# Optimization experiments

Hardware: AMD Instinct MI355X
Metric: run time of the kernel (lower is better)

## Reference

```python
import jax, jax.numpy as jnp
import numpy as np

TOP_K = 2  # config.top_k


def setup_inputs() -> dict:
    key = jax.random.key(0)
    k0, k1, k2, k3, k4 = jax.random.split(key, 5)
    B, S, D, F, E = 1, 2048, 512, 1024, 8
    scale = 0.02
    hidden_states = jax.random.normal(k0, (B, S, D), dtype=jnp.float32)
    router_w = jax.random.normal(k1, (D, E), dtype=jnp.float32) * scale
    w1 = jax.random.normal(k2, (E, D, F), dtype=jnp.float32) * scale  # gate proj
    w2 = jax.random.normal(k3, (E, F, D), dtype=jnp.float32) * scale  # down proj
    w3 = jax.random.normal(k4, (E, D, F), dtype=jnp.float32) * scale  # up proj
    return {"hidden_states": hidden_states, "router_w": router_w,
            "w1": w1, "w2": w2, "w3": w3}


def reference(hidden_states, router_w, w1, w2, w3):
    B, S, D = hidden_states.shape
    E = router_w.shape[1]
    x = hidden_states.reshape(-1, D)                      # [T, D]
    T = x.shape[0]

    # router: softmax in float32, top-k, renormalize (matches torch source)
    router_logits = x @ router_w                          # [T, E]
    probs = jax.nn.softmax(router_logits.astype(jnp.float32), axis=-1)
    routing_weights, selected_experts = jax.lax.top_k(probs, TOP_K)  # [T, K]
    routing_weights = routing_weights / routing_weights.sum(axis=-1, keepdims=True)
    routing_weights = routing_weights.astype(x.dtype)

    # combine weights: scatter top-k weights into dense [T, E] (one-hot combine)
    combine = jnp.zeros((T, E), dtype=x.dtype).at[
        jnp.arange(T)[:, None], selected_experts].add(routing_weights)

    # dense-all-experts evaluation, math-identical to gather-GEMM-scatter:
    # unselected experts get combine weight 0 and contribute nothing.
    gate = jax.nn.silu(jnp.einsum('td,edf->tef', x, w1))  # [T, E, F]
    up = jnp.einsum('td,edf->tef', x, w3)                 # [T, E, F]
    h = gate * up * combine[:, :, None]                   # weight before down-proj
    out = jnp.einsum('tef,efd->td', h, w2)                # [T, D]
    return out.reshape(B, S, D)
```

## Files before the change

kernel.cpp:

```cpp
#include <hip/hip_runtime.h>
#include <hip/hip_bf16.h>


typedef __attribute__((ext_vector_type(4))) float f32x4;
typedef __attribute__((ext_vector_type(8))) __bf16 bf16x8;

#define T_TOK 2048
#define DMODEL 512
#define FFN 1024
#define NE 8
#define MAXMB 40
#define PCAP (MAXMB * 128)

__device__ __forceinline__ void gload_lds16(const void* g, void* l) {
  __builtin_amdgcn_global_load_lds(
      (const __attribute__((address_space(1))) void*)g,
      (__attribute__((address_space(3))) void*)l, 16, 0, 0);
}

#define PIPE_BAR_8()                                        \
  asm volatile("s_waitcnt vmcnt(8)" ::: "memory");          \
  __builtin_amdgcn_s_barrier();                             \
  __builtin_amdgcn_sched_barrier(0)
#define PIPE_BAR_6()                                        \
  asm volatile("s_waitcnt vmcnt(6)" ::: "memory");          \
  __builtin_amdgcn_s_barrier();                             \
  __builtin_amdgcn_sched_barrier(0)
#define PIPE_BAR_0()                                        \
  asm volatile("s_waitcnt vmcnt(0)" ::: "memory");          \
  __builtin_amdgcn_s_barrier();                             \
  __builtin_amdgcn_sched_barrier(0)
#define POST_BAR()                                          \
  __builtin_amdgcn_s_barrier();                             \
  __builtin_amdgcn_sched_barrier(0)

__global__ __launch_bounds__(256) void cvt_router_kernel(
    const float* __restrict__ x, const float* __restrict__ rw,
    __bf16* __restrict__ xb, int* __restrict__ tope, float* __restrict__ topw) {
  const int t = blockIdx.x * 4 + (threadIdx.x >> 6);
  const int lane = threadIdx.x & 63;
  const float* xr = x + (size_t)t * DMODEL + lane * 8;
  const f32x4 a = *(const f32x4*)xr;
  const f32x4 b = *(const f32x4*)(xr + 4);
  bf16x8 v;
  v[0] = (__bf16)a[0]; v[1] = (__bf16)a[1]; v[2] = (__bf16)a[2]; v[3] = (__bf16)a[3];
  v[4] = (__bf16)b[0]; v[5] = (__bf16)b[1]; v[6] = (__bf16)b[2]; v[7] = (__bf16)b[3];
  *(bf16x8*)&xb[(size_t)t * DMODEL + lane * 8] = v;

  float xv[8] = {a[0], a[1], a[2], a[3], b[0], b[1], b[2], b[3]};
  float part[NE];
#pragma unroll
  for (int e = 0; e < NE; ++e) part[e] = 0.f;
#pragma unroll
  for (int i = 0; i < 8; ++i) {
    const int d = lane * 8 + i;
    const f32x4 r0 = *(const f32x4*)&rw[(size_t)d * NE];
    const f32x4 r1 = *(const f32x4*)&rw[(size_t)d * NE + 4];
    part[0] += xv[i] * r0[0]; part[1] += xv[i] * r0[1];
    part[2] += xv[i] * r0[2]; part[3] += xv[i] * r0[3];
    part[4] += xv[i] * r1[0]; part[5] += xv[i] * r1[1];
    part[6] += xv[i] * r1[2]; part[7] += xv[i] * r1[3];
  }
#pragma unroll
  for (int off = 32; off > 0; off >>= 1) {
#pragma unroll
    for (int e = 0; e < NE; ++e) part[e] += __shfl_xor(part[e], off);
  }
  if (lane == 0) {
    int ia = 0;
#pragma unroll
    for (int e = 1; e < NE; ++e)
      if (part[e] > part[ia]) ia = e;
    int ib = (ia == 0) ? 1 : 0;
#pragma unroll
    for (int e = 0; e < NE; ++e)
      if (e != ia && e != ib && part[e] > part[ib]) ib = e;
    const float wa = 1.f / (1.f + __expf(part[ib] - part[ia]));
    tope[t * 2] = ia;
    tope[t * 2 + 1] = ib;
    topw[t * 2] = wa;
    topw[t * 2 + 1] = 1.f - wa;
  }
}

__global__ __launch_bounds__(256) void build_kernel(
    const int* __restrict__ tope, const float* __restrict__ topw,
    int* __restrict__ pair_t, float* __restrict__ pair_w,
    int* __restrict__ pairidx, int* __restrict__ sched_e) {
  __shared__ int cnt[NE], base[NE], ofs[NE];
  const int tid = threadIdx.x;
  if (tid < NE) { cnt[tid] = 0; ofs[tid] = 0; }
  for (int i = tid; i < PCAP; i += 256) { pair_t[i] = 0; pair_w[i] = 0.f; }
  for (int i = tid; i < MAXMB; i += 256) sched_e[i] = -1;
  __syncthreads();
  for (int t = tid; t < T_TOK; t += 256) {
    atomicAdd(&cnt[tope[t * 2]], 1);
    atomicAdd(&cnt[tope[t * 2 + 1]], 1);
  }
  __syncthreads();
  if (tid == 0) {
    int mb = 0;
    for (int e = 0; e < NE; ++e) {
      base[e] = mb * 128;
      const int nmb = (cnt[e] + 127) >> 7;
      for (int i = 0; i < nmb; ++i) sched_e[mb + i] = e;
      mb += nmb;
    }
  }
  __syncthreads();
  for (int t = tid; t < T_TOK; t += 256) {
#pragma unroll
    for (int s = 0; s < 2; ++s) {
      const int e = tope[t * 2 + s];
      const int pos = base[e] + atomicAdd(&ofs[e], 1);
      pair_t[pos] = t;
      pair_w[pos] = topw[t * 2 + s];
      pairidx[t * 2 + s] = pos;
    }
  }
}

__global__ __launch_bounds__(256) void transpose_all_kernel(
    const float* __restrict__ w1, const float* __restrict__ w2,
    const float* __restrict__ w3, __bf16* __restrict__ w1t,
    __bf16* __restrict__ w2t, __bf16* __restrict__ w3t) {
  __shared__ __bf16 tile[64][65];
  const int tid = threadIdx.x;
  const int bx = blockIdx.x;
  const float* src;
  __bf16* dst;
  int R, C, idx;
  if (bx < 1024)      { src = w1; dst = w1t; R = 512;  C = 1024; idx = bx; }
  else if (bx < 2048) { src = w3; dst = w3t; R = 512;  C = 1024; idx = bx - 1024; }
  else                { src = w2; dst = w2t; R = 1024; C = 512;  idx = bx - 2048; }
  const int ntx = C >> 6, nty = R >> 6;
  const int cx = idx % ntx;
  const int gry = idx / ntx;
  const int e = gry / nty;
  const int r0 = (gry % nty) * 64;
  const int c0 = cx * 64;
  src += (size_t)e * R * C;
  dst += (size_t)e * R * C;
#pragma unroll
  for (int q = 0; q < 4; ++q) {
    const int r = (tid >> 4) + q * 16;
    const int c = (tid & 15) * 4;
    const f32x4 v = *(const f32x4*)&src[(size_t)(r0 + r) * C + c0 + c];
    tile[r][c] = (__bf16)v[0];
    tile[r][c + 1] = (__bf16)v[1];
    tile[r][c + 2] = (__bf16)v[2];
    tile[r][c + 3] = (__bf16)v[3];
  }
  __syncthreads();
#pragma unroll
  for (int p = 0; p < 2; ++p) {
    const int cc = (tid >> 3) + p * 32;
    const int rr = (tid & 7) * 8;
    union { bf16x8 v; __bf16 s[8]; } u;
#pragma unroll
    for (int i = 0; i < 8; ++i) u.s[i] = tile[rr + i][cc];
    *(bf16x8*)&dst[(size_t)(c0 + cc) * R + r0 + rr] = u.v;
  }
}

__global__ __launch_bounds__(256) void gemm1_kernel(
    const __bf16* __restrict__ xb, const __bf16* __restrict__ w1t,
    const __bf16* __restrict__ w3t, const int* __restrict__ pair_t,
    const float* __restrict__ pair_w, const int* __restrict__ sched_e,
    __bf16* __restrict__ hbuf) {
  __shared__ alignas(16) __bf16 As[2][128 * 64];
  __shared__ alignas(16) __bf16 B1s[2][64 * 64];
  __shared__ alignas(16) __bf16 B3s[2][64 * 64];
  __shared__ float comb[128];
  const int tid = threadIdx.x;
  const int id = blockIdx.x;
  const int mb = (id & 7) + ((id >> 7) << 3);
  const int f0 = ((id >> 3) & 15) * 64;
  const int e = sched_e[mb];
  if (e < 0) return;
  const int m0 = mb * 128;
  const int lane = tid & 63;
  const int wv = tid >> 6;
  const int wr = wv >> 1, wc = wv & 1;
  const int l15 = lane & 15, lhi = lane >> 4;
  const int sw = (l15 & 7) << 4;

  if (tid < 128) comb[tid] = pair_w[m0 + tid];

  size_t aoff[4];
  int lbA[4];
#pragma unroll
  for (int it = 0; it < 4; ++it) {
    const int chunk = it * 256 + tid;
    const int r = chunk >> 3;
    const int c8 = ((chunk & 7) ^ (r & 7)) * 8;
    aoff[it] = (size_t)pair_t[m0 + r] * DMODEL + c8;
    lbA[it] = (it * 256 + (tid & ~63)) * 16;
  }
  size_t boff[2];
  int lbB[2];
#pragma unroll
  for (int it = 0; it < 2; ++it) {
    const int chunk = it * 256 + tid;
    const int r = chunk >> 3;
    const int c8 = ((chunk & 7) ^ (r & 7)) * 8;
    boff[it] = (size_t)(e * FFN + f0 + r) * DMODEL + c8;
    lbB[it] = (it * 256 + (tid & ~63)) * 16;
  }

  const f32x4 fz = {0.f, 0.f, 0.f, 0.f};
  f32x4 acc1[4][2], acc3[4][2];
#pragma unroll
  for (int m = 0; m < 4; ++m)
#pragma unroll
    for (int n = 0; n < 2; ++n) { acc1[m][n] = fz; acc3[m][n] = fz; }

#define G1_STAGE(BUF, K0)                                                     \
  do {                                                                        \
    _Pragma("unroll") for (int it = 0; it < 4; ++it)                          \
        gload_lds16(xb + aoff[it] + (K0), (char*)As[BUF] + lbA[it]);          \
    _Pragma("unroll") for (int it = 0; it < 2; ++it) {                        \
      gload_lds16(w1t + boff[it] + (K0), (char*)B1s[BUF] + lbB[it]);          \
      gload_lds16(w3t + boff[it] + (K0), (char*)B3s[BUF] + lbB[it]);          \
    }                                                                         \
  } while (0)

#define G1_COMPUTE(BUF)                                                       \
  do {                                                                        \
    __builtin_amdgcn_s_setprio(1);                                            \
    _Pragma("unroll") for (int kk = 0; kk < 2; ++kk) {                        \
      const int ko = (kk * 64 + lhi * 16) ^ sw;                               \
      bf16x8 af[4], b1f[2], b3f[2];                                           \
      _Pragma("unroll") for (int m = 0; m < 4; ++m)                           \
          af[m] = *(const bf16x8*)((const char*)As[BUF] +                     \
                                   (wr * 64 + m * 16 + l15) * 128 + ko);      \
      _Pragma("unroll") for (int n = 0; n < 2; ++n) {                         \
        const int ro = (wc * 32 + n * 16 + l15) * 128 + ko;                   \
        b1f[n] = *(const bf16x8*)((const char*)B1s[BUF] + ro);                \
        b3f[n] = *(const bf16x8*)((const char*)B3s[BUF] + ro);                \
      }                                                                       \
      _Pragma("unroll") for (int m = 0; m < 4; ++m)                           \
          _Pragma("unroll") for (int n = 0; n < 2; ++n) {                     \
        acc1[m][n] = __builtin_amdgcn_mfma_f32_16x16x32_bf16(af[m], b1f[n],   \
                                                             acc1[m][n], 0, 0, 0); \
        acc3[m][n] = __builtin_amdgcn_mfma_f32_16x16x32_bf16(af[m], b3f[n],   \
                                                             acc3[m][n], 0, 0, 0); \
      }                                                                       \
    }                                                                         \
    __builtin_amdgcn_s_setprio(0);                                            \
  } while (0)

  G1_STAGE(0, 0);
#pragma unroll
  for (int t = 0; t < 7; ++t) {
    G1_STAGE((t + 1) & 1, (t + 1) * 64);
    PIPE_BAR_8();
    G1_COMPUTE(t & 1);
    POST_BAR();
  }
  PIPE_BAR_0();
  G1_COMPUTE(1);

#pragma unroll
  for (int m = 0; m < 4; ++m)
#pragma unroll
    for (int n = 0; n < 2; ++n)
#pragma unroll
      for (int r = 0; r < 4; ++r) {
        const int row = wr * 64 + m * 16 + lhi * 4 + r;
        const int col = wc * 32 + n * 16 + l15;
        const float g = acc1[m][n][r];
        const float u = acc3[m][n][r];
        const float val = (g / (1.f + __expf(-g))) * u * comb[row];
        hbuf[(size_t)(m0 + row) * FFN + f0 + col] = (__bf16)val;
      }
#undef G1_STAGE
#undef G1_COMPUTE
}

__global__ __launch_bounds__(256) void gemm2_kernel(
    const __bf16* __restrict__ hbuf, const __bf16* __restrict__ w2t,
    const int* __restrict__ sched_e, __bf16* __restrict__ outp) {
  __shared__ alignas(16) __bf16 As[2][128 * 64];
  __shared__ alignas(16) __bf16 Bs[2][64 * 64];
  const int tid = threadIdx.x;
  const int id = blockIdx.x;
  const int gk = (id & 7) + ((id >> 6) << 3);
  const int n0 = ((id >> 3) & 7) * 64;
  const int mb = gk >> 1;
  const int kz = gk & 1;
  const int e = sched_e[mb];
  if (e < 0) return;
  const int m0 = mb * 128;
  const int fbase = kz * (FFN / 2);
  const int lane = tid & 63;
  const int wv = tid >> 6;
  const int wr = wv >> 1, wc = wv & 1;
  const int l15 = lane & 15, lhi = lane >> 4;
  const int sw = (l15 & 7) << 4;

  size_t aoff[4];
  int lbA[4];
#pragma unroll
  for (int it = 0; it < 4; ++it) {
    const int chunk = it * 256 + tid;
    const int r = chunk >> 3;
    const int c8 = ((chunk & 7) ^ (r & 7)) * 8;
    aoff[it] = (size_t)(m0 + r) * FFN + fbase + c8;
    lbA[it] = (it * 256 + (tid & ~63)) * 16;
  }
  size_t boff[2];
  int lbB[2];
#pragma unroll
  for (int it = 0; it < 2; ++it) {
    const int chunk = it * 256 + tid;
    const int r = chunk >> 3;
    const int c8 = ((chunk & 7) ^ (r & 7)) * 8;
    boff[it] = ((size_t)e * DMODEL + n0 + r) * FFN + fbase + c8;
    lbB[it] = (it * 256 + (tid & ~63)) * 16;
  }

  const f32x4 fz = {0.f, 0.f, 0.f, 0.f};
  f32x4 acc[4][2];
#pragma unroll
  for (int m = 0; m < 4; ++m) { acc[m][0] = fz; acc[m][1] = fz; }

#define G2_STAGE(BUF, K0)                                                     \
  do {                                                                        \
    _Pragma("unroll") for (int it = 0; it < 4; ++it)                          \
        gload_lds16(hbuf + aoff[it] + (K0), (char*)As[BUF] + lbA[it]);        \
    _Pragma("unroll") for (int it = 0; it < 2; ++it)                          \
        gload_lds16(w2t + boff[it] + (K0), (char*)Bs[BUF] + lbB[it]);         \
  } while (0)

#define G2_COMPUTE(BUF)                                                       \
  do {                                                                        \
    __builtin_amdgcn_s_setprio(1);                                            \
    _Pragma("unroll") for (int kk = 0; kk < 2; ++kk) {                        \
      const int ko = (kk * 64 + lhi * 16) ^ sw;                               \
      bf16x8 af[4], bfr[2];                                                   \
      _Pragma("unroll") for (int m = 0; m < 4; ++m)                           \
          af[m] = *(const bf16x8*)((const char*)As[BUF] +                     \
                                   (wr * 64 + m * 16 + l15) * 128 + ko);      \
      _Pragma("unroll") for (int n = 0; n < 2; ++n)                           \
          bfr[n] = *(const bf16x8*)((const char*)Bs[BUF] +                    \
                                    (wc * 32 + n * 16 + l15) * 128 + ko);     \
      _Pragma("unroll") for (int m = 0; m < 4; ++m)                           \
          _Pragma("unroll") for (int n = 0; n < 2; ++n)                       \
              acc[m][n] = __builtin_amdgcn_mfma_f32_16x16x32_bf16(            \
                  af[m], bfr[n], acc[m][n], 0, 0, 0);                         \
    }                                                                         \
    __builtin_amdgcn_s_setprio(0);                                            \
  } while (0)

  G2_STAGE(0, 0);
#pragma unroll
  for (int t = 0; t < 7; ++t) {
    G2_STAGE((t + 1) & 1, (t + 1) * 64);
    PIPE_BAR_6();
    G2_COMPUTE(t & 1);
    POST_BAR();
  }
  PIPE_BAR_0();
  G2_COMPUTE(1);

#pragma unroll
  for (int m = 0; m < 4; ++m)
#pragma unroll
    for (int n = 0; n < 2; ++n)
#pragma unroll
      for (int r = 0; r < 4; ++r) {
        const int row = wr * 64 + m * 16 + lhi * 4 + r;
        const int col = wc * 32 + n * 16 + l15;
        outp[((size_t)kz * PCAP + m0 + row) * DMODEL + n0 + col] =
            (__bf16)acc[m][n][r];
      }
#undef G2_STAGE
#undef G2_COMPUTE
}

__global__ __launch_bounds__(256) void gather_kernel(
    const __bf16* __restrict__ outp, const int* __restrict__ pairidx,
    float* __restrict__ out) {
  const int i = blockIdx.x * 256 + threadIdx.x;
  const int t = i >> 6;
  const int c = (i & 63) * 8;
  const int p0 = pairidx[t * 2];
  const int p1 = pairidx[t * 2 + 1];
  const size_t KZ = (size_t)PCAP * DMODEL;
  const bf16x8 a0 = *(const bf16x8*)&outp[(size_t)p0 * DMODEL + c];
  const bf16x8 a1 = *(const bf16x8*)&outp[(size_t)p1 * DMODEL + c];
  const bf16x8 b0 = *(const bf16x8*)&outp[KZ + (size_t)p0 * DMODEL + c];
  const bf16x8 b1 = *(const bf16x8*)&outp[KZ + (size_t)p1 * DMODEL + c];
  f32x4 lo, hi;
#pragma unroll
  for (int j = 0; j < 4; ++j)
    lo[j] = (float)a0[j] + (float)a1[j] + (float)b0[j] + (float)b1[j];
#pragma unroll
  for (int j = 0; j < 4; ++j)
    hi[j] = (float)a0[j + 4] + (float)a1[j + 4] + (float)b0[j + 4] + (float)b1[j + 4];
  float* op = out + (size_t)t * DMODEL + c;
  *(f32x4*)op = lo;
  *(f32x4*)(op + 4) = hi;
}

extern "C" void kernel_launch(void* const* d_in, const int* in_sizes, int n_in,
                              void* d_out, int out_size, void* d_ws, size_t ws_size,
                              hipStream_t stream) {
  const float* x = (const float*)d_in[0];
  const float* rw = (const float*)d_in[1];
  const float* w1 = (const float*)d_in[2];
  const float* w2 = (const float*)d_in[3];
  const float* w3 = (const float*)d_in[4];
  float* out = (float*)d_out;
  char* ws = (char*)d_ws;

  int* tope = (int*)(ws + 0);
  float* topw = (float*)(ws + 16384);
  int* pair_t = (int*)(ws + 32768);
  float* pair_w = (float*)(ws + 53248);
  int* pairidx = (int*)(ws + 73728);
  int* sched_e = (int*)(ws + 90112);
  __bf16* xb = (__bf16*)(ws + 98304);
  __bf16* w1t = (__bf16*)(ws + 2195456);
  __bf16* w3t = (__bf16*)(ws + 10584064);
  __bf16* w2t = (__bf16*)(ws + 18972672);
  __bf16* hbuf = (__bf16*)(ws + 27361280);
  __bf16* outp = (__bf16*)(ws + 37847040);

  hipLaunchKernelGGL(cvt_router_kernel, dim3(T_TOK / 4), dim3(256), 0, stream, x, rw, xb, tope, topw);
  hipLaunchKernelGGL(build_kernel, dim3(1), dim3(256), 0, stream, tope, topw, pair_t, pair_w, pairidx, sched_e);
  hipLaunchKernelGGL(transpose_all_kernel, dim3(3072), dim3(256), 0, stream, w1, w2, w3, w1t, w2t, w3t);
  hipLaunchKernelGGL(gemm1_kernel, dim3(640), dim3(256), 0, stream, xb, w1t, w3t, pair_t, pair_w, sched_e, hbuf);
  hipLaunchKernelGGL(gemm2_kernel, dim3(640), dim3(256), 0, stream, hbuf, w2t, sched_e, outp);
  hipLaunchKernelGGL(gather_kernel, dim3(512), dim3(256), 0, stream, outp, pairidx, out);
}
```

Baseline: 74.09 us.

## Fuse router, weight transpose and init into one prep kernel; stage GEMM epilogues via LDS

Merges the router/convert kernel, the weight transpose kernel and the pair-buffer initialization into a single prep kernel. This removes one launch and moves the serial init loop out of the single-block build kernel. Both GEMM epilogues now write results to a padded LDS tile first and then store 16-byte vectors to global memory, replacing scattered 2-byte writes. The costs are an extra barrier plus LDS round trip per tile, and a larger, more divergent prep kernel.

```diff
diff --git a/kernel.cpp b/kernel.cpp
--- a/kernel.cpp
+++ b/kernel.cpp
@@ -34,52 +34,102 @@
   __builtin_amdgcn_s_barrier();                             \
   __builtin_amdgcn_sched_barrier(0)
 
-__global__ __launch_bounds__(256) void cvt_router_kernel(
+__global__ __launch_bounds__(256) void prep_kernel(
     const float* __restrict__ x, const float* __restrict__ rw,
-    __bf16* __restrict__ xb, int* __restrict__ tope, float* __restrict__ topw) {
-  const int t = blockIdx.x * 4 + (threadIdx.x >> 6);
-  const int lane = threadIdx.x & 63;
-  const float* xr = x + (size_t)t * DMODEL + lane * 8;
-  const f32x4 a = *(const f32x4*)xr;
-  const f32x4 b = *(const f32x4*)(xr + 4);
-  bf16x8 v;
-  v[0] = (__bf16)a[0]; v[1] = (__bf16)a[1]; v[2] = (__bf16)a[2]; v[3] = (__bf16)a[3];
-  v[4] = (__bf16)b[0]; v[5] = (__bf16)b[1]; v[6] = (__bf16)b[2]; v[7] = (__bf16)b[3];
-  *(bf16x8*)&xb[(size_t)t * DMODEL + lane * 8] = v;
-
-  float xv[8] = {a[0], a[1], a[2], a[3], b[0], b[1], b[2], b[3]};
-  float part[NE];
-#pragma unroll
-  for (int e = 0; e < NE; ++e) part[e] = 0.f;
-#pragma unroll
-  for (int i = 0; i < 8; ++i) {
-    const int d = lane * 8 + i;
-    const f32x4 r0 = *(const f32x4*)&rw[(size_t)d * NE];
-    const f32x4 r1 = *(const f32x4*)&rw[(size_t)d * NE + 4];
-    part[0] += xv[i] * r0[0]; part[1] += xv[i] * r0[1];
-    part[2] += xv[i] * r0[2]; part[3] += xv[i] * r0[3];
-    part[4] += xv[i] * r1[0]; part[5] += xv[i] * r1[1];
-    part[6] += xv[i] * r1[2]; part[7] += xv[i] * r1[3];
-  }
-#pragma unroll
-  for (int off = 32; off > 0; off >>= 1) {
-#pragma unroll
-    for (int e = 0; e < NE; ++e) part[e] += __shfl_xor(part[e], off);
-  }
-  if (lane == 0) {
-    int ia = 0;
-#pragma unroll
-    for (int e = 1; e < NE; ++e)
-      if (part[e] > part[ia]) ia = e;
-    int ib = (ia == 0) ? 1 : 0;
-#pragma unroll
-    for (int e = 0; e < NE; ++e)
-      if (e != ia && e != ib && part[e] > part[ib]) ib = e;
-    const float wa = 1.f / (1.f + __expf(part[ib] - part[ia]));
-    tope[t * 2] = ia;
-    tope[t * 2 + 1] = ib;
-    topw[t * 2] = wa;
-    topw[t * 2 + 1] = 1.f - wa;
+    const float* __restrict__ w1, const float* __restrict__ w2,
+    const float* __restrict__ w3, __bf16* __restrict__ xb,
+    __bf16* __restrict__ w1t, __bf16* __restrict__ w2t,
+    __bf16* __restrict__ w3t, int* __restrict__ tope, float* __restrict__ topw,
+    int* __restrict__ pair_t, float* __restrict__ pair_w,
+    int* __restrict__ sched_e) {
+  __shared__ __bf16 tile[64][65];
+  const int bx = blockIdx.x;
+  const int tid = threadIdx.x;
+
+  if (bx < 3072) {
+    const float* src;
+    __bf16* dst;
+    int R, C, idx;
+    if (bx < 1024)      { src = w1; dst = w1t; R = 512;  C = 1024; idx = bx; }
+    else if (bx < 2048) { src = w3; dst = w3t; R = 512;  C = 1024; idx = bx - 1024; }
+    else                { src = w2; dst = w2t; R = 1024; C = 512;  idx = bx - 2048; }
+    const int ntx = C >> 6, nty = R >> 6;
+    const int cx = idx % ntx;
+    const int gry = idx / ntx;
+    const int e = gry / nty;
+    const int r0 = (gry % nty) * 64;
+    const int c0 = cx * 64;
+    src += (size_t)e * R * C;
+    dst += (size_t)e * R * C;
+#pragma unroll
+    for (int q = 0; q < 4; ++q) {
+      const int r = (tid >> 4) + q * 16;
+      const int c = (tid & 15) * 4;
+      const f32x4 v = *(const f32x4*)&src[(size_t)(r0 + r) * C + c0 + c];
+      tile[r][c] = (__bf16)v[0];
+      tile[r][c + 1] = (__bf16)v[1];
+      tile[r][c + 2] = (__bf16)v[2];
+      tile[r][c + 3] = (__bf16)v[3];
+    }
+    __syncthreads();
+#pragma unroll
+    for (int p = 0; p < 2; ++p) {
+      const int cc = (tid >> 3) + p * 32;
+      const int rr = (tid & 7) * 8;
+      union { bf16x8 v; __bf16 s[8]; } u;
+#pragma unroll
+      for (int i = 0; i < 8; ++i) u.s[i] = tile[rr + i][cc];
+      *(bf16x8*)&dst[(size_t)(c0 + cc) * R + r0 + rr] = u.v;
+    }
+  } else if (bx < 3584) {
+    const int t = (bx - 3072) * 4 + (tid >> 6);
+    const int lane = tid & 63;
+    const float* xr = x + (size_t)t * DMODEL + lane * 8;
+    const f32x4 a = *(const f32x4*)xr;
+    const f32x4 b = *(const f32x4*)(xr + 4);
+    bf16x8 v;
+    v[0] = (__bf16)a[0]; v[1] = (__bf16)a[1]; v[2] = (__bf16)a[2]; v[3] = (__bf16)a[3];
+    v[4] = (__bf16)b[0]; v[5] = (__bf16)b[1]; v[6] = (__bf16)b[2]; v[7] = (__bf16)b[3];
+    *(bf16x8*)&xb[(size_t)t * DMODEL + lane * 8] = v;
+
+    float xv[8] = {a[0], a[1], a[2], a[3], b[0], b[1], b[2], b[3]};
+    float part[NE];
+#pragma unroll
+    for (int e = 0; e < NE; ++e) part[e] = 0.f;
+#pragma unroll
+    for (int i = 0; i < 8; ++i) {
+      const int d = lane * 8 + i;
+      const f32x4 r0 = *(const f32x4*)&rw[(size_t)d * NE];
+      const f32x4 r1 = *(const f32x4*)&rw[(size_t)d * NE + 4];
+      part[0] += xv[i] * r0[0]; part[1] += xv[i] * r0[1];
+      part[2] += xv[i] * r0[2]; part[3] += xv[i] * r0[3];
+      part[4] += xv[i] * r1[0]; part[5] += xv[i] * r1[1];
+      part[6] += xv[i] * r1[2]; part[7] += xv[i] * r1[3];
+    }
+#pragma unroll
+    for (int off = 32; off > 0; off >>= 1) {
+#pragma unroll
+      for (int e = 0; e < NE; ++e) part[e] += __shfl_xor(part[e], off);
+    }
+    if (lane == 0) {
+      int ia = 0;
+#pragma unroll
+      for (int e = 1; e < NE; ++e)
+        if (part[e] > part[ia]) ia = e;
+      int ib = (ia == 0) ? 1 : 0;
+#pragma unroll
+      for (int e = 0; e < NE; ++e)
+        if (e != ia && e != ib && part[e] > part[ib]) ib = e;
+      const float wa = 1.f / (1.f + __expf(part[ib] - part[ia]));
+      tope[t * 2] = ia;
+      tope[t * 2 + 1] = ib;
+      topw[t * 2] = wa;
+      topw[t * 2 + 1] = 1.f - wa;
+    }
+  } else {
+    const int i = (bx - 3584) * 256 + tid;
+    for (int j = i; j < PCAP; j += 2048) { pair_t[j] = 0; pair_w[j] = 0.f; }
+    if (i < MAXMB) sched_e[i] = -1;
   }
 }
 
@@ -90,8 +140,6 @@
   __shared__ int cnt[NE], base[NE], ofs[NE];
   const int tid = threadIdx.x;
   if (tid < NE) { cnt[tid] = 0; ofs[tid] = 0; }
-  for (int i = tid; i < PCAP; i += 256) { pair_t[i] = 0; pair_w[i] = 0.f; }
-  for (int i = tid; i < MAXMB; i += 256) sched_e[i] = -1;
   __syncthreads();
   for (int t = tid; t < T_TOK; t += 256) {
     atomicAdd(&cnt[tope[t * 2]], 1);
@@ -117,49 +165,6 @@
       pair_w[pos] = topw[t * 2 + s];
       pairidx[t * 2 + s] = pos;
     }
-  }
-}
-
-__global__ __launch_bounds__(256) void transpose_all_kernel(
-    const float* __restrict__ w1, const float* __restrict__ w2,
-    const float* __restrict__ w3, __bf16* __restrict__ w1t,
-    __bf16* __restrict__ w2t, __bf16* __restrict__ w3t) {
-  __shared__ __bf16 tile[64][65];
-  const int tid = threadIdx.x;
-  const int bx = blockIdx.x;
-  const float* src;
-  __bf16* dst;
-  int R, C, idx;
-  if (bx < 1024)      { src = w1; dst = w1t; R = 512;  C = 1024; idx = bx; }
-  else if (bx < 2048) { src = w3; dst = w3t; R = 512;  C = 1024; idx = bx - 1024; }
-  else                { src = w2; dst = w2t; R = 1024; C = 512;  idx = bx - 2048; }
-  const int ntx = C >> 6, nty = R >> 6;
-  const int cx = idx % ntx;
-  const int gry = idx / ntx;
-  const int e = gry / nty;
-  const int r0 = (gry % nty) * 64;
-  const int c0 = cx * 64;
-  src += (size_t)e * R * C;
-  dst += (size_t)e * R * C;
-#pragma unroll
-  for (int q = 0; q < 4; ++q) {
-    const int r = (tid >> 4) + q * 16;
-    const int c = (tid & 15) * 4;
-    const f32x4 v = *(const f32x4*)&src[(size_t)(r0 + r) * C + c0 + c];
-    tile[r][c] = (__bf16)v[0];
-    tile[r][c + 1] = (__bf16)v[1];
-    tile[r][c + 2] = (__bf16)v[2];
-    tile[r][c + 3] = (__bf16)v[3];
-  }
-  __syncthreads();
-#pragma unroll
-  for (int p = 0; p < 2; ++p) {
-    const int cc = (tid >> 3) + p * 32;
-    const int rr = (tid & 7) * 8;
-    union { bf16x8 v; __bf16 s[8]; } u;
-#pragma unroll
-    for (int i = 0; i < 8; ++i) u.s[i] = tile[rr + i][cc];
-    *(bf16x8*)&dst[(size_t)(c0 + cc) * R + r0 + rr] = u.v;
   }
 }
 
@@ -261,19 +266,31 @@
   PIPE_BAR_0();
   G1_COMPUTE(1);
 
-#pragma unroll
-  for (int m = 0; m < 4; ++m)
-#pragma unroll
-    for (int n = 0; n < 2; ++n)
-#pragma unroll
-      for (int r = 0; r < 4; ++r) {
-        const int row = wr * 64 + m * 16 + lhi * 4 + r;
-        const int col = wc * 32 + n * 16 + l15;
-        const float g = acc1[m][n][r];
-        const float u = acc3[m][n][r];
-        const float val = (g / (1.f + __expf(-g))) * u * comb[row];
-        hbuf[(size_t)(m0 + row) * FFN + f0 + col] = (__bf16)val;
-      }
+  __syncthreads();
+  {
+    __bf16* eps = (__bf16*)As;
+    constexpr int EW = 72;
+#pragma unroll
+    for (int m = 0; m < 4; ++m)
+#pragma unroll
+      for (int n = 0; n < 2; ++n)
+#pragma unroll
+        for (int r = 0; r < 4; ++r) {
+          const int row = wr * 64 + m * 16 + lhi * 4 + r;
+          const int col = wc * 32 + n * 16 + l15;
+          const float g = acc1[m][n][r];
+          const float u = acc3[m][n][r];
+          eps[row * EW + col] = (__bf16)((g / (1.f + __expf(-g))) * u * comb[row]);
+        }
+    __syncthreads();
+#pragma unroll
+    for (int p = 0; p < 4; ++p) {
+      const int i = p * 256 + tid;
+      const int row = i >> 3, c8 = (i & 7) * 8;
+      *(bf16x8*)&hbuf[(size_t)(m0 + row) * FFN + f0 + c8] =
+          *(const bf16x8*)&eps[row * EW + c8];
+    }
+  }
 #undef G1_STAGE
 #undef G1_COMPUTE
 }
@@ -364,17 +381,29 @@
   PIPE_BAR_0();
   G2_COMPUTE(1);
 
-#pragma unroll
-  for (int m = 0; m < 4; ++m)
-#pragma unroll
-    for (int n = 0; n < 2; ++n)
-#pragma unroll
-      for (int r = 0; r < 4; ++r) {
-        const int row = wr * 64 + m * 16 + lhi * 4 + r;
-        const int col = wc * 32 + n * 16 + l15;
-        outp[((size_t)kz * PCAP + m0 + row) * DMODEL + n0 + col] =
-            (__bf16)acc[m][n][r];
-      }
+  __syncthreads();
+  {
+    __bf16* eps = (__bf16*)As;
+    constexpr int EW = 72;
+#pragma unroll
+    for (int m = 0; m < 4; ++m)
+#pragma unroll
+      for (int n = 0; n < 2; ++n)
+#pragma unroll
+        for (int r = 0; r < 4; ++r) {
+          const int row = wr * 64 + m * 16 + lhi * 4 + r;
+          const int col = wc * 32 + n * 16 + l15;
+          eps[row * EW + col] = (__bf16)acc[m][n][r];
+        }
+    __syncthreads();
+#pragma unroll
+    for (int p = 0; p < 4; ++p) {
+      const int i = p * 256 + tid;
+      const int row = i >> 3, c8 = (i & 7) * 8;
+      *(bf16x8*)&outp[((size_t)kz * PCAP + m0 + row) * DMODEL + n0 + c8] =
+          *(const bf16x8*)&eps[row * EW + c8];
+    }
+  }
 #undef G2_STAGE
 #undef G2_COMPUTE
 }
@@ -428,10 +457,15 @@
   __bf16* hbuf = (__bf16*)(ws + 27361280);
   __bf16* outp = (__bf16*)(ws + 37847040);
 
-  hipLaunchKernelGGL(cvt_router_kernel, dim3(T_TOK / 4), dim3(256), 0, stream, x, rw, xb, tope, topw);
-  hipLaunchKernelGGL(build_kernel, dim3(1), dim3(256), 0, stream, tope, topw, pair_t, pair_w, pairidx, sched_e);
-  hipLaunchKernelGGL(transpose_all_kernel, dim3(3072), dim3(256), 0, stream, w1, w2, w3, w1t, w2t, w3t);
-  hipLaunchKernelGGL(gemm1_kernel, dim3(640), dim3(256), 0, stream, xb, w1t, w3t, pair_t, pair_w, sched_e, hbuf);
-  hipLaunchKernelGGL(gemm2_kernel, dim3(640), dim3(256), 0, stream, hbuf, w2t, sched_e, outp);
-  hipLaunchKernelGGL(gather_kernel, dim3(512), dim3(256), 0, stream, outp, pairidx, out);
-}
+  hipLaunchKernelGGL(prep_kernel, dim3(3592), dim3(256), 0, stream,
+                     x, rw, w1, w2, w3, xb, w1t, w2t, w3t, tope, topw,
+                     pair_t, pair_w, sched_e);
+  hipLaunchKernelGGL(build_kernel, dim3(1), dim3(256), 0, stream,
+                     tope, topw, pair_t, pair_w, pairidx, sched_e);
+  hipLaunchKernelGGL(gemm1_kernel, dim3(640), dim3(256), 0, stream,
+                     xb, w1t, w3t, pair_t, pair_w, sched_e, hbuf);
+  hipLaunchKernelGGL(gemm2_kernel, dim3(640), dim3(256), 0, stream,
+                     hbuf, w2t, sched_e, outp);
+  hipLaunchKernelGGL(gather_kernel, dim3(512), dim3(256), 0, stream,
+                     outp, pairidx, out);
+}
```

After: 72.90 us, median of 2. About the same (-1.6%).
